# Optimization experiments

Hardware: AMD Instinct MI355X
Metric: run time of the kernel (lower is better)

Reference implementation:

```python
import jax, jax.numpy as jnp
import numpy as np

B, N, IN_DIM, HEADS, OUT_DIM = 8, 2048, 256, 4, 64
NEG_SLOPE = 0.2


def setup_inputs() -> dict:
    key = jax.random.key(0)
    k_h, k_w, k_as, k_ad = jax.random.split(key, 4)
    h = jax.random.normal(k_h, (B, N, IN_DIM), dtype=jnp.float32)
    # xavier-uniform-like scales
    w_lim = float(np.sqrt(6.0 / (IN_DIM + HEADS * OUT_DIM)))
    a_lim = float(np.sqrt(6.0 / (HEADS + OUT_DIM)))
    W = jax.random.uniform(k_w, (IN_DIM, HEADS * OUT_DIM), jnp.float32, -w_lim, w_lim)
    a_src = jax.random.uniform(k_as, (HEADS, OUT_DIM), jnp.float32, -a_lim, a_lim)
    a_dst = jax.random.uniform(k_ad, (HEADS, OUT_DIM), jnp.float32, -a_lim, a_lim)
    bias = jnp.zeros((HEADS * OUT_DIM,), jnp.float32)
    mask = jnp.ones((B, N), dtype=bool)
    return {"h": h, "W": W, "a_src": a_src, "a_dst": a_dst, "bias": bias, "mask": mask}


def reference(h, W, a_src, a_dst, bias, mask):
    Bn, Nn, _ = h.shape
    Hh, Dd = a_src.shape
    # Wh: [B, H, N, D]
    Wh = (h @ W).reshape(Bn, Nn, Hh, Dd).transpose(0, 2, 1, 3)
    el = jnp.einsum("bhnd,hd->bhn", Wh, a_src)  # [B,H,N]
    er = jnp.einsum("bhnd,hd->bhn", Wh, a_dst)  # [B,H,N]
    # e[b,h,i,j] = leaky_relu(el[b,h,i] + er[b,h,j])
    e = jax.nn.leaky_relu(el[..., :, None] + er[..., None, :], NEG_SLOPE)
    e = jnp.where(mask[:, None, None, :], e, jnp.float32(-1e9))
    alpha = jax.nn.softmax(e, axis=-1)  # over source nodes j (dropout=0/eval)
    h_prime = jnp.einsum("bhij,bhjd->bhid", alpha, Wh)  # [B,H,N,D]
    h_prime = h_prime.transpose(0, 2, 1, 3).reshape(Bn, Nn, Hh * Dd)  # concat heads
    return h_prime + bias
```

## Files before the change

kernel.cpp:

```cpp
#include <hip/hip_runtime.h>
#include <math.h>

#define B_   8
#define N_   2048
#define IN_  256
#define H_   4
#define D_   64
#define C_   256
#define M_   (B_*N_)
#define NEG  0.2f
#define LOG2E 1.4426950408889634f

typedef short bf16x8 __attribute__((ext_vector_type(8)));
typedef float f32x4  __attribute__((ext_vector_type(4)));

__device__ inline ushort f32_to_bf16_rne(float x) {
    union { float f; unsigned u; } c; c.f = x;
    unsigned u = c.u + 0x7FFFu + ((c.u >> 16) & 1u);
    return (ushort)(u >> 16);
}
__device__ inline float bf16_hi_to_f32(ushort u) {
    union { unsigned u; float f; } c; c.u = ((unsigned)u) << 16;
    return c.f;
}
__device__ inline void split8(const float v[8], bf16x8* hi, bf16x8* lo) {
    union { bf16x8 v; ushort u[8]; } H, L;
    #pragma unroll
    for (int j = 0; j < 8; j++) {
        ushort hb = f32_to_bf16_rne(v[j]);
        H.u[j] = hb;
        L.u[j] = f32_to_bf16_rne(v[j] - bf16_hi_to_f32(hb));
    }
    *hi = H.v; *lo = L.v;
}

__global__ __launch_bounds__(256) void wprep_kernel(const float* __restrict__ W,
                                                    ushort* __restrict__ Wt_hi,
                                                    ushort* __restrict__ Wt_lo) {
    const int t = threadIdx.x, blk = blockIdx.x;
    ushort his[4], los[4];
    #pragma unroll
    for (int kk = 0; kk < 4; kk++) {
        float v = W[(blk * 4 + kk) * 256 + t];
        ushort hi = f32_to_bf16_rne(v);
        his[kk] = hi;
        los[kk] = f32_to_bf16_rne(v - bf16_hi_to_f32(hi));
    }
    *(uint2*)&Wt_hi[(size_t)t * 256 + blk * 4] =
        make_uint2(((uint)his[0]) | (((uint)his[1]) << 16), ((uint)his[2]) | (((uint)his[3]) << 16));
    *(uint2*)&Wt_lo[(size_t)t * 256 + blk * 4] =
        make_uint2(((uint)los[0]) | (((uint)los[1]) << 16), ((uint)los[2]) | (((uint)los[3]) << 16));
}

#define BP 264
#define EP 136

__global__ __launch_bounds__(256, 2) void gemm_fused(const float* __restrict__ h,
                                                     const ushort* __restrict__ Wt_hi,
                                                     const ushort* __restrict__ Wt_lo,
                                                     const float* __restrict__ a_src,
                                                     const float* __restrict__ a_dst,
                                                     ushort* __restrict__ Wht,
                                                     float* __restrict__ Ee,
                                                     float* __restrict__ Ff,
                                                     float* __restrict__ Gg) {
    __shared__ ushort Bs_h[64 * BP], Bs_l[64 * BP];

    const int t = threadIdx.x;
    const int m0 = blockIdx.x * 128;
    const int nb = blockIdx.y;
    const int b  = m0 >> 11;
    const int wid = t >> 6, lane = t & 63;
    const int c16 = lane & 15, quad = lane >> 4;

    {
        const int c = t >> 2, kq = t & 3;
        const ushort* sh = Wt_hi + (size_t)(nb * 64 + c) * 256 + kq * 64;
        const ushort* sl = Wt_lo + (size_t)(nb * 64 + c) * 256 + kq * 64;
        ushort* dh = &Bs_h[c * BP + kq * 64];
        ushort* dl = &Bs_l[c * BP + kq * 64];
        #pragma unroll
        for (int q = 0; q < 8; q++) {
            *(uint4*)(dh + q * 8) = *(const uint4*)(sh + q * 8);
            *(uint4*)(dl + q * 8) = *(const uint4*)(sl + q * 8);
        }
    }

    const int row0 = m0 + wid * 32 + c16;
    const float* hp0 = h + (size_t)row0 * 256 + quad * 8;
    const float* hp1 = hp0 + 16 * 256;

    float4 p0a = *(const float4*)hp0, p0b = *(const float4*)(hp0 + 4);
    float4 p1a = *(const float4*)hp1, p1b = *(const float4*)(hp1 + 4);

    __syncthreads();

    f32x4 acc[2][4] = {};
    for (int k0 = 0; k0 < 256; k0 += 32) {
        float v0[8] = {p0a.x, p0a.y, p0a.z, p0a.w, p0b.x, p0b.y, p0b.z, p0b.w};
        float v1[8] = {p1a.x, p1a.y, p1a.z, p1a.w, p1b.x, p1b.y, p1b.z, p1b.w};
        if (k0 < 224) {
            p0a = *(const float4*)(hp0 + k0 + 32); p0b = *(const float4*)(hp0 + k0 + 36);
            p1a = *(const float4*)(hp1 + k0 + 32); p1b = *(const float4*)(hp1 + k0 + 36);
        }
        bf16x8 ah0, al0, ah1, al1;
        split8(v0, &ah0, &al0);
        split8(v1, &ah1, &al1);
        #pragma unroll
        for (int fc = 0; fc < 4; fc++) {
            bf16x8 bhf = *(const bf16x8*)&Bs_h[(fc * 16 + c16) * BP + k0 + quad * 8];
            bf16x8 blf = *(const bf16x8*)&Bs_l[(fc * 16 + c16) * BP + k0 + quad * 8];
            acc[0][fc] = __builtin_amdgcn_mfma_f32_16x16x32_bf16(ah0, bhf, acc[0][fc], 0, 0, 0);
            acc[0][fc] = __builtin_amdgcn_mfma_f32_16x16x32_bf16(al0, bhf, acc[0][fc], 0, 0, 0);
            acc[0][fc] = __builtin_amdgcn_mfma_f32_16x16x32_bf16(ah0, blf, acc[0][fc], 0, 0, 0);
            acc[1][fc] = __builtin_amdgcn_mfma_f32_16x16x32_bf16(ah1, bhf, acc[1][fc], 0, 0, 0);
            acc[1][fc] = __builtin_amdgcn_mfma_f32_16x16x32_bf16(al1, bhf, acc[1][fc], 0, 0, 0);
            acc[1][fc] = __builtin_amdgcn_mfma_f32_16x16x32_bf16(ah1, blf, acc[1][fc], 0, 0, 0);
        }
    }

    {
        float avs[4], avd[4];
        #pragma unroll
        for (int fc = 0; fc < 4; fc++) {
            avs[fc] = a_src[nb * 64 + fc * 16 + c16];
            avd[fc] = a_dst[nb * 64 + fc * 16 + c16];
        }
        float ds[2][4] = {}, dd[2][4] = {};
        #pragma unroll
        for (int rw = 0; rw < 2; rw++)
            #pragma unroll
            for (int r = 0; r < 4; r++)
                #pragma unroll
                for (int fc = 0; fc < 4; fc++) {
                    ds[rw][r] += acc[rw][fc][r] * avs[fc];
                    dd[rw][r] += acc[rw][fc][r] * avd[fc];
                }
        #pragma unroll
        for (int off = 1; off < 16; off <<= 1)
            #pragma unroll
            for (int rw = 0; rw < 2; rw++)
                #pragma unroll
                for (int r = 0; r < 4; r++) {
                    ds[rw][r] += __shfl_xor(ds[rw][r], off);
                    dd[rw][r] += __shfl_xor(dd[rw][r], off);
                }
        if (c16 == 0) {
            #pragma unroll
            for (int rw = 0; rw < 2; rw++)
                #pragma unroll
                for (int r = 0; r < 4; r++) {
                    int m = m0 + wid * 32 + rw * 16 + quad * 4 + r;
                    int idx = (b * 4 + nb) * N_ + (m & 2047);
                    float ee = ds[rw][r] * LOG2E;
                    float rr = dd[rw][r] * LOG2E;
                    Ee[idx] = __builtin_amdgcn_exp2f(rr);
                    Ff[idx] = __builtin_amdgcn_exp2f(NEG * rr);
                    Gg[idx] = __builtin_amdgcn_exp2f(-0.8f * ee);
                }
        }
    }

    __syncthreads();
    ushort* Es = Bs_h;
    #pragma unroll
    for (int rw = 0; rw < 2; rw++) {
        const int nloc = wid * 32 + rw * 16 + quad * 4;
        #pragma unroll
        for (int fc = 0; fc < 4; fc++) {
            const int d = fc * 16 + c16;
            uint2 pk = make_uint2(
                ((uint)f32_to_bf16_rne(acc[rw][fc][0])) | (((uint)f32_to_bf16_rne(acc[rw][fc][1])) << 16),
                ((uint)f32_to_bf16_rne(acc[rw][fc][2])) | (((uint)f32_to_bf16_rne(acc[rw][fc][3])) << 16));
            *(uint2*)&Es[d * EP + nloc] = pk;
        }
    }
    __syncthreads();
    {
        const int d = t >> 2, ch = t & 3;
        ushort* dst = Wht + ((size_t)(b * 4 + nb) * 64 + d) * N_ + (m0 & 2047) + ch * 32;
        const ushort* srcl = &Es[d * EP + ch * 32];
        #pragma unroll
        for (int q = 0; q < 4; q++)
            *(uint4*)(dst + q * 8) = *(const uint4*)(srcl + q * 8);
    }
}

#define TPA 80

__global__ __launch_bounds__(256, 2) void attn_kernel(const ushort* __restrict__ Wht,
                                                      const float* __restrict__ Ee,
                                                      const float* __restrict__ Ff,
                                                      const float* __restrict__ Gg,
                                                      const float* __restrict__ bias,
                                                      float* __restrict__ out) {
    __shared__ ushort Whs[2][64 * TPA];
    __shared__ float E_s[2][64], F_s[2][64];
    const int t = threadIdx.x;
    const int bh = blockIdx.x, b = bh >> 2, hh = bh & 3;
    const int wid = t >> 6, lane = t & 63;
    const int c16 = lane & 15, quad = lane >> 4;
    const int ibase = blockIdx.y * 128 + wid * 32;
    const int sd = t >> 3, sch = t & 7;

    float Gi[2];
    #pragma unroll
    for (int g = 0; g < 2; g++) Gi[g] = Gg[bh * N_ + ibase + g * 16 + c16];

    f32x4 acc[2][4] = {};
    f32x4 den[2] = {};
    const bf16x8 ones = {0x3F80, 0x3F80, 0x3F80, 0x3F80,
                         0x3F80, 0x3F80, 0x3F80, 0x3F80};
    const ushort* WhtB = Wht + (size_t)bh * 64 * N_;
    const float* Eb = Ee + (size_t)bh * N_;
    const float* Fb = Ff + (size_t)bh * N_;

    uint4 w0 = *(const uint4*)(WhtB + (size_t)sd * N_ + sch * 8);
    uint4 w1 = *(const uint4*)(WhtB + (size_t)(sd + 32) * N_ + sch * 8);
    float ev_e = 0.f, ev_f = 0.f;
    if (t < 64) { ev_e = Eb[t]; ev_f = Fb[t]; }

    for (int jt = 0; jt < 32; jt++) {
        const int buf = jt & 1;
        *(uint4*)&Whs[buf][sd * TPA + sch * 8]        = w0;
        *(uint4*)&Whs[buf][(sd + 32) * TPA + sch * 8] = w1;
        if (t < 64) { E_s[buf][t] = ev_e; F_s[buf][t] = ev_f; }
        if (jt < 31) {
            const int j1 = (jt + 1) * 64;
            w0 = *(const uint4*)(WhtB + (size_t)sd * N_ + j1 + sch * 8);
            w1 = *(const uint4*)(WhtB + (size_t)(sd + 32) * N_ + j1 + sch * 8);
            if (t < 64) { ev_e = Eb[j1 + t]; ev_f = Fb[j1 + t]; }
        }
        __syncthreads();
        #pragma unroll
        for (int ks = 0; ks < 2; ks++) {
            const int jb = ks * 32 + quad * 8;
            float4 e0 = *(const float4*)&E_s[buf][jb];
            float4 e1 = *(const float4*)&E_s[buf][jb + 4];
            float4 f0 = *(const float4*)&F_s[buf][jb];
            float4 f1 = *(const float4*)&F_s[buf][jb + 4];
            float E8[8] = {e0.x, e0.y, e0.z, e0.w, e1.x, e1.y, e1.z, e1.w};
            float F8[8] = {f0.x, f0.y, f0.z, f0.w, f1.x, f1.y, f1.z, f1.w};
            bf16x8 bfr[4];
            #pragma unroll
            for (int fd = 0; fd < 4; fd++)
                bfr[fd] = *(const bf16x8*)&Whs[buf][(fd * 16 + c16) * TPA + jb];
            #pragma unroll
            for (int g = 0; g < 2; g++) {
                const float gi = Gi[g];
                uint uu[8];
                #pragma unroll
                for (int j = 0; j < 8; j++) {
                    float q = fmaxf(E8[j], gi * F8[j]);
                    uu[j] = __float_as_uint(q) + 0x8000u;
                }
                union { bf16x8 v; uint u[4]; } af;
                #pragma unroll
                for (int j = 0; j < 4; j++)
                    af.u[j] = __builtin_amdgcn_perm(uu[2 * j + 1], uu[2 * j], 0x07060302u);
                #pragma unroll
                for (int fd = 0; fd < 4; fd++)
                    acc[g][fd] = __builtin_amdgcn_mfma_f32_16x16x32_bf16(af.v, bfr[fd], acc[g][fd], 0, 0, 0);
                den[g] = __builtin_amdgcn_mfma_f32_16x16x32_bf16(af.v, ones, den[g], 0, 0, 0);
            }
        }
    }

    float bl[4];
    #pragma unroll
    for (int fd = 0; fd < 4; fd++) bl[fd] = bias[hh * 64 + fd * 16 + c16];
    #pragma unroll
    for (int g = 0; g < 2; g++)
        #pragma unroll
        for (int r = 0; r < 4; r++) {
            int i = ibase + g * 16 + quad * 4 + r;
            float inv = 1.0f / den[g][r];
            float* dst = out + (size_t)(b * N_ + i) * C_ + hh * 64;
            #pragma unroll
            for (int fd = 0; fd < 4; fd++)
                dst[fd * 16 + c16] = acc[g][fd][r] * inv + bl[fd];
        }
}

extern "C" void kernel_launch(void* const* d_in, const int* in_sizes, int n_in,
                              void* d_out, int out_size, void* d_ws, size_t ws_size,
                              hipStream_t stream) {
    const float* h     = (const float*)d_in[0];
    const float* W     = (const float*)d_in[1];
    const float* a_src = (const float*)d_in[2];
    const float* a_dst = (const float*)d_in[3];
    const float* bias  = (const float*)d_in[4];
    float* out = (float*)d_out;

    ushort* Wt_hi = (ushort*)d_ws;
    ushort* Wt_lo = Wt_hi + 256 * 256;
    ushort* Wht   = Wt_lo + 256 * 256;
    float*  Ee    = (float*)(Wht + (size_t)M_ * C_);
    float*  Ff    = Ee + 32 * N_;
    float*  Gg    = Ff + 32 * N_;

    wprep_kernel<<<64, 256, 0, stream>>>(W, Wt_hi, Wt_lo);
    gemm_fused<<<dim3(M_ / 128, 4), 256, 0, stream>>>(h, Wt_hi, Wt_lo, a_src, a_dst,
                                                      Wht, Ee, Ff, Gg);
    attn_kernel<<<dim3(32, 16), 256, 0, stream>>>(Wht, Ee, Ff, Gg, bias, out);
}
```

Before: 122.8 us.

## Replace dense attention with sort-and-prefix-sum evaluation of separable leaky-relu softmax

```diff
diff --git a/kernel.cpp b/kernel.cpp
--- a/kernel.cpp
+++ b/kernel.cpp
@@ -53,17 +53,15 @@
 }
 
 #define BP 264
-#define EP 136
 
 __global__ __launch_bounds__(256, 2) void gemm_fused(const float* __restrict__ h,
                                                      const ushort* __restrict__ Wt_hi,
                                                      const ushort* __restrict__ Wt_lo,
                                                      const float* __restrict__ a_src,
                                                      const float* __restrict__ a_dst,
-                                                     ushort* __restrict__ Wht,
-                                                     float* __restrict__ Ee,
-                                                     float* __restrict__ Ff,
-                                                     float* __restrict__ Gg) {
+                                                     float* __restrict__ Wh,
+                                                     float* __restrict__ eL,
+                                                     float* __restrict__ rL) {
     __shared__ ushort Bs_h[64 * BP], Bs_l[64 * BP];
 
     const int t = threadIdx.x;
@@ -152,134 +150,233 @@
                 for (int r = 0; r < 4; r++) {
                     int m = m0 + wid * 32 + rw * 16 + quad * 4 + r;
                     int idx = (b * 4 + nb) * N_ + (m & 2047);
-                    float ee = ds[rw][r] * LOG2E;
-                    float rr = dd[rw][r] * LOG2E;
-                    Ee[idx] = __builtin_amdgcn_exp2f(rr);
-                    Ff[idx] = __builtin_amdgcn_exp2f(NEG * rr);
-                    Gg[idx] = __builtin_amdgcn_exp2f(-0.8f * ee);
+                    eL[idx] = ds[rw][r] * LOG2E;
+                    rL[idx] = dd[rw][r] * LOG2E;
                 }
         }
     }
 
+    #pragma unroll
+    for (int rw = 0; rw < 2; rw++)
+        #pragma unroll
+        for (int r = 0; r < 4; r++) {
+            int n = m0 + wid * 32 + rw * 16 + quad * 4 + r;
+            float* dst = Wh + (size_t)n * 256 + nb * 64;
+            #pragma unroll
+            for (int fc = 0; fc < 4; fc++)
+                dst[fc * 16 + c16] = acc[rw][fc][r];
+        }
+}
+
+__global__ __launch_bounds__(256) void sort_kernel(const float* __restrict__ rL,
+                                                   float* __restrict__ r_srt,
+                                                   int* __restrict__ perm,
+                                                   float* __restrict__ E_srt,
+                                                   float* __restrict__ F_srt) {
+    __shared__ float key[2048];
+    __shared__ int   idx[2048];
+    const int bh = blockIdx.x, t = threadIdx.x;
+    for (int s = t; s < 2048; s += 256) { key[s] = rL[bh * 2048 + s]; idx[s] = s; }
     __syncthreads();
-    ushort* Es = Bs_h;
-    #pragma unroll
-    for (int rw = 0; rw < 2; rw++) {
-        const int nloc = wid * 32 + rw * 16 + quad * 4;
-        #pragma unroll
-        for (int fc = 0; fc < 4; fc++) {
-            const int d = fc * 16 + c16;
-            uint2 pk = make_uint2(
-                ((uint)f32_to_bf16_rne(acc[rw][fc][0])) | (((uint)f32_to_bf16_rne(acc[rw][fc][1])) << 16),
-                ((uint)f32_to_bf16_rne(acc[rw][fc][2])) | (((uint)f32_to_bf16_rne(acc[rw][fc][3])) << 16));
-            *(uint2*)&Es[d * EP + nloc] = pk;
-        }
-    }
+    for (int k = 2; k <= 2048; k <<= 1) {
+        for (int j = k >> 1; j > 0; j >>= 1) {
+            for (int s = t; s < 2048; s += 256) {
+                int p = s ^ j;
+                if (p > s) {
+                    bool up = ((s & k) == 0);
+                    float a = key[s], bq = key[p];
+                    bool sw = up ? (a > bq) : (a < bq);
+                    if (sw) {
+                        key[s] = bq; key[p] = a;
+                        int ia = idx[s]; idx[s] = idx[p]; idx[p] = ia;
+                    }
+                }
+            }
+            __syncthreads();
+        }
+    }
+    for (int s = t; s < 2048; s += 256) {
+        float rv = key[s];
+        r_srt[bh * 2048 + s] = rv;
+        perm[bh * 2048 + s]  = idx[s];
+        E_srt[bh * 2048 + s] = __builtin_amdgcn_exp2f(rv);
+        F_srt[bh * 2048 + s] = __builtin_amdgcn_exp2f(NEG * rv);
+    }
+}
+
+__global__ __launch_bounds__(256) void chunksum_kernel(const float* __restrict__ Wh,
+                                                       const int* __restrict__ perm,
+                                                       const float* __restrict__ E_srt,
+                                                       const float* __restrict__ F_srt,
+                                                       float* __restrict__ chunkF,
+                                                       float* __restrict__ chunkE,
+                                                       float* __restrict__ chunk_sf,
+                                                       float* __restrict__ chunk_se) {
+    const int bh = blockIdx.x;
+    const int b = bh >> 2, hh = bh & 3;
+    const int w = threadIdx.x >> 6, lane = threadIdx.x & 63;
+    const int ch = blockIdx.y * 4 + w;
+    const int j0 = ch * 32;
+
+    float fv = 0.f, ev = 0.f; int pv = 0;
+    if (lane < 32) {
+        fv = F_srt[bh * 2048 + j0 + lane];
+        ev = E_srt[bh * 2048 + j0 + lane];
+        pv = perm[bh * 2048 + j0 + lane];
+    }
+    float v[32];
+    #pragma unroll
+    for (int jj = 0; jj < 32; jj++) {
+        int pj = __shfl(pv, jj);
+        v[jj] = Wh[((size_t)(b * 2048 + pj)) * 256 + hh * 64 + lane];
+    }
+    float aF = 0.f, aE = 0.f, sf = 0.f, se = 0.f;
+    #pragma unroll
+    for (int jj = 0; jj < 32; jj++) {
+        float fj = __shfl(fv, jj), ej = __shfl(ev, jj);
+        aF += fj * v[jj]; aE += ej * v[jj];
+        sf += fj; se += ej;
+    }
+    size_t o = ((size_t)bh * 64 + ch) * 64 + lane;
+    chunkF[o] = aF; chunkE[o] = aE;
+    if (lane == 0) { chunk_sf[bh * 64 + ch] = sf; chunk_se[bh * 64 + ch] = se; }
+}
+
+__global__ __launch_bounds__(64) void scan_kernel(const float* __restrict__ chunkF,
+                                                  const float* __restrict__ chunkE,
+                                                  const float* __restrict__ chunk_sf,
+                                                  const float* __restrict__ chunk_se,
+                                                  float* __restrict__ offF,
+                                                  float* __restrict__ offE,
+                                                  float* __restrict__ offF_s,
+                                                  float* __restrict__ offE_s,
+                                                  float* __restrict__ PF,
+                                                  float* __restrict__ SES,
+                                                  float* __restrict__ pf_s,
+                                                  float* __restrict__ ses_s) {
+    const int bh = blockIdx.x, d = threadIdx.x;
+    float accF = 0.f, sF = 0.f;
+    for (int c = 0; c < 64; c++) {
+        size_t o = ((size_t)bh * 64 + c) * 64 + d;
+        offF[o] = accF;
+        if (d == 0) offF_s[bh * 64 + c] = sF;
+        accF += chunkF[o];
+        sF += chunk_sf[bh * 64 + c];
+    }
+    float accE = 0.f, sE = 0.f;
+    for (int c = 63; c >= 0; c--) {
+        size_t o = ((size_t)bh * 64 + c) * 64 + d;
+        offE[o] = accE;
+        if (d == 0) offE_s[bh * 64 + c] = sE;
+        accE += chunkE[o];
+        sE += chunk_se[bh * 64 + c];
+    }
+    PF[((size_t)bh * 2049 + 2048) * 64 + d]  = accF;
+    SES[((size_t)bh * 2049 + 2048) * 64 + d] = 0.0f;
+    if (d == 0) { pf_s[bh * 2049 + 2048] = sF; ses_s[bh * 2049 + 2048] = 0.0f; }
+}
+
+__global__ __launch_bounds__(64) void emit_kernel(const float* __restrict__ Wh,
+                                                  const int* __restrict__ perm,
+                                                  const float* __restrict__ E_srt,
+                                                  const float* __restrict__ F_srt,
+                                                  const float* __restrict__ offF,
+                                                  const float* __restrict__ offE,
+                                                  const float* __restrict__ offF_s,
+                                                  const float* __restrict__ offE_s,
+                                                  float* __restrict__ PF,
+                                                  float* __restrict__ SES,
+                                                  float* __restrict__ pf_s,
+                                                  float* __restrict__ ses_s) {
+    const int bh = blockIdx.x, ch = blockIdx.y;
+    const int b = bh >> 2, hh = bh & 3;
+    const int d = threadIdx.x;
+    const int j0 = ch * 32;
+
+    float fv = 0.f, ev = 0.f; int pv = 0;
+    if (d < 32) {
+        fv = F_srt[bh * 2048 + j0 + d];
+        ev = E_srt[bh * 2048 + j0 + d];
+        pv = perm[bh * 2048 + j0 + d];
+    }
+    float v[32];
+    #pragma unroll
+    for (int jj = 0; jj < 32; jj++) {
+        int pj = __shfl(pv, jj);
+        v[jj] = Wh[((size_t)(b * 2048 + pj)) * 256 + hh * 64 + d];
+    }
+    float accF = offF[((size_t)bh * 64 + ch) * 64 + d];
+    float sF   = offF_s[bh * 64 + ch];
+    #pragma unroll
+    for (int jj = 0; jj < 32; jj++) {
+        float fj = __shfl(fv, jj);
+        size_t ro = ((size_t)bh * 2049 + j0 + jj) * 64 + d;
+        PF[ro] = accF;
+        if (d == 0) pf_s[bh * 2049 + j0 + jj] = sF;
+        accF += fj * v[jj];
+        sF += fj;
+    }
+    float accE = offE[((size_t)bh * 64 + ch) * 64 + d];
+    float sE   = offE_s[bh * 64 + ch];
+    #pragma unroll
+    for (int jj = 31; jj >= 0; jj--) {
+        float ej = __shfl(ev, jj);
+        accE += ej * v[jj];
+        sE += ej;
+        size_t ro = ((size_t)bh * 2049 + j0 + jj) * 64 + d;
+        SES[ro] = accE;
+        if (d == 0) ses_s[bh * 2049 + j0 + jj] = sE;
+    }
+}
+
+__global__ __launch_bounds__(256) void final_kernel(const float* __restrict__ eL,
+                                                    const float* __restrict__ r_srt,
+                                                    const float* __restrict__ PF,
+                                                    const float* __restrict__ SES,
+                                                    const float* __restrict__ pf_s,
+                                                    const float* __restrict__ ses_s,
+                                                    const float* __restrict__ bias,
+                                                    float* __restrict__ out) {
+    __shared__ float r_sh[2048];
+    __shared__ int   t_sh[64];
+    __shared__ float g_sh[64];
+    const int bh = blockIdx.x, ig = blockIdx.y;
+    const int b = bh >> 2, hh = bh & 3;
+    const int t = threadIdx.x;
+
+    for (int s = t; s < 2048; s += 256) r_sh[s] = r_srt[bh * 2048 + s];
     __syncthreads();
-    {
-        const int d = t >> 2, ch = t & 3;
-        ushort* dst = Wht + ((size_t)(b * 4 + nb) * 64 + d) * N_ + (m0 & 2047) + ch * 32;
-        const ushort* srcl = &Es[d * EP + ch * 32];
-        #pragma unroll
-        for (int q = 0; q < 4; q++)
-            *(uint4*)(dst + q * 8) = *(const uint4*)(srcl + q * 8);
-    }
-}
-
-#define TPA 80
-
-__global__ __launch_bounds__(256, 2) void attn_kernel(const ushort* __restrict__ Wht,
-                                                      const float* __restrict__ Ee,
-                                                      const float* __restrict__ Ff,
-                                                      const float* __restrict__ Gg,
-                                                      const float* __restrict__ bias,
-                                                      float* __restrict__ out) {
-    __shared__ ushort Whs[2][64 * TPA];
-    __shared__ float E_s[2][64], F_s[2][64];
-    const int t = threadIdx.x;
-    const int bh = blockIdx.x, b = bh >> 2, hh = bh & 3;
-    const int wid = t >> 6, lane = t & 63;
-    const int c16 = lane & 15, quad = lane >> 4;
-    const int ibase = blockIdx.y * 128 + wid * 32;
-    const int sd = t >> 3, sch = t & 7;
-
-    float Gi[2];
-    #pragma unroll
-    for (int g = 0; g < 2; g++) Gi[g] = Gg[bh * N_ + ibase + g * 16 + c16];
-
-    f32x4 acc[2][4] = {};
-    f32x4 den[2] = {};
-    const bf16x8 ones = {0x3F80, 0x3F80, 0x3F80, 0x3F80,
-                         0x3F80, 0x3F80, 0x3F80, 0x3F80};
-    const ushort* WhtB = Wht + (size_t)bh * 64 * N_;
-    const float* Eb = Ee + (size_t)bh * N_;
-    const float* Fb = Ff + (size_t)bh * N_;
-
-    uint4 w0 = *(const uint4*)(WhtB + (size_t)sd * N_ + sch * 8);
-    uint4 w1 = *(const uint4*)(WhtB + (size_t)(sd + 32) * N_ + sch * 8);
-    float ev_e = 0.f, ev_f = 0.f;
-    if (t < 64) { ev_e = Eb[t]; ev_f = Fb[t]; }
-
-    for (int jt = 0; jt < 32; jt++) {
-        const int buf = jt & 1;
-        *(uint4*)&Whs[buf][sd * TPA + sch * 8]        = w0;
-        *(uint4*)&Whs[buf][(sd + 32) * TPA + sch * 8] = w1;
-        if (t < 64) { E_s[buf][t] = ev_e; F_s[buf][t] = ev_f; }
-        if (jt < 31) {
-            const int j1 = (jt + 1) * 64;
-            w0 = *(const uint4*)(WhtB + (size_t)sd * N_ + j1 + sch * 8);
-            w1 = *(const uint4*)(WhtB + (size_t)(sd + 32) * N_ + j1 + sch * 8);
-            if (t < 64) { ev_e = Eb[j1 + t]; ev_f = Fb[j1 + t]; }
-        }
-        __syncthreads();
-        #pragma unroll
-        for (int ks = 0; ks < 2; ks++) {
-            const int jb = ks * 32 + quad * 8;
-            float4 e0 = *(const float4*)&E_s[buf][jb];
-            float4 e1 = *(const float4*)&E_s[buf][jb + 4];
-            float4 f0 = *(const float4*)&F_s[buf][jb];
-            float4 f1 = *(const float4*)&F_s[buf][jb + 4];
-            float E8[8] = {e0.x, e0.y, e0.z, e0.w, e1.x, e1.y, e1.z, e1.w};
-            float F8[8] = {f0.x, f0.y, f0.z, f0.w, f1.x, f1.y, f1.z, f1.w};
-            bf16x8 bfr[4];
-            #pragma unroll
-            for (int fd = 0; fd < 4; fd++)
-                bfr[fd] = *(const bf16x8*)&Whs[buf][(fd * 16 + c16) * TPA + jb];
-            #pragma unroll
-            for (int g = 0; g < 2; g++) {
-                const float gi = Gi[g];
-                uint uu[8];
-                #pragma unroll
-                for (int j = 0; j < 8; j++) {
-                    float q = fmaxf(E8[j], gi * F8[j]);
-                    uu[j] = __float_as_uint(q) + 0x8000u;
-                }
-                union { bf16x8 v; uint u[4]; } af;
-                #pragma unroll
-                for (int j = 0; j < 4; j++)
-                    af.u[j] = __builtin_amdgcn_perm(uu[2 * j + 1], uu[2 * j], 0x07060302u);
-                #pragma unroll
-                for (int fd = 0; fd < 4; fd++)
-                    acc[g][fd] = __builtin_amdgcn_mfma_f32_16x16x32_bf16(af.v, bfr[fd], acc[g][fd], 0, 0, 0);
-                den[g] = __builtin_amdgcn_mfma_f32_16x16x32_bf16(af.v, ones, den[g], 0, 0, 0);
-            }
-        }
-    }
-
-    float bl[4];
-    #pragma unroll
-    for (int fd = 0; fd < 4; fd++) bl[fd] = bias[hh * 64 + fd * 16 + c16];
-    #pragma unroll
-    for (int g = 0; g < 2; g++)
-        #pragma unroll
-        for (int r = 0; r < 4; r++) {
-            int i = ibase + g * 16 + quad * 4 + r;
-            float inv = 1.0f / den[g][r];
-            float* dst = out + (size_t)(b * N_ + i) * C_ + hh * 64;
-            #pragma unroll
-            for (int fd = 0; fd < 4; fd++)
-                dst[fd * 16 + c16] = acc[g][fd][r] * inv + bl[fd];
-        }
+    if (t < 64) {
+        int i = ig * 64 + t;
+        float e = eL[bh * 2048 + i];
+        float target = -e;
+        int lo = 0, hi = 2048;
+        while (lo < hi) {
+            int mid = (lo + hi) >> 1;
+            if (r_sh[mid] < target) lo = mid + 1; else hi = mid;
+        }
+        t_sh[t] = lo;
+        g_sh[t] = __builtin_amdgcn_exp2f(-0.8f * e);
+    }
+    __syncthreads();
+
+    const int w = t >> 6, lane = t & 63;
+    const float bl = bias[hh * 64 + lane];
+    #pragma unroll 4
+    for (int q = 0; q < 16; q++) {
+        int il = w * 16 + q;
+        int ti = t_sh[il];
+        float G = g_sh[il];
+        size_t base = ((size_t)bh * 2049 + ti) * 64 + lane;
+        float pf  = PF[base];
+        float ses = SES[base];
+        float dpf  = pf_s[bh * 2049 + ti];
+        float dses = ses_s[bh * 2049 + ti];
+        float num = G * pf + ses;
+        float den = G * dpf + dses;
+        int i = ig * 64 + il;
+        out[((size_t)(b * 2048 + i)) * 256 + hh * 64 + lane] = num / den + bl;
+    }
 }
 
 extern "C" void kernel_launch(void* const* d_in, const int* in_sizes, int n_in,
@@ -292,15 +389,40 @@
     const float* bias  = (const float*)d_in[4];
     float* out = (float*)d_out;
 
-    ushort* Wt_hi = (ushort*)d_ws;
-    ushort* Wt_lo = Wt_hi + 256 * 256;
-    ushort* Wht   = Wt_lo + 256 * 256;
-    float*  Ee    = (float*)(Wht + (size_t)M_ * C_);
-    float*  Ff    = Ee + 32 * N_;
-    float*  Gg    = Ff + 32 * N_;
+    float* Wh       = (float*)d_ws;
+    float* eL       = Wh + (size_t)M_ * C_;
+    float* rL       = eL + 32 * N_;
+    float* r_srt    = rL + 32 * N_;
+    float* E_srt    = r_srt + 32 * N_;
+    float* F_srt    = E_srt + 32 * N_;
+    float* chunkF   = F_srt + 32 * N_;
+    float* chunkE   = chunkF + 32 * 64 * 64;
+    float* chunk_sf = chunkE + 32 * 64 * 64;
+    float* chunk_se = chunk_sf + 32 * 64;
+    float* offF     = chunk_se + 32 * 64;
+    float* offE     = offF + 32 * 64 * 64;
+    float* offF_s   = offE + 32 * 64 * 64;
+    float* offE_s   = offF_s + 32 * 64;
+    float* PF       = offE_s + 32 * 64;
+    float* SES      = PF + (size_t)32 * 2049 * 64;
+    float* pf_s     = SES + (size_t)32 * 2049 * 64;
+    float* ses_s    = pf_s + 32 * 2049;
+    int*   perm     = (int*)(ses_s + 32 * 2049);
+    ushort* Wt_hi   = (ushort*)(perm + 32 * N_);
+    ushort* Wt_lo   = Wt_hi + 256 * 256;
 
     wprep_kernel<<<64, 256, 0, stream>>>(W, Wt_hi, Wt_lo);
     gemm_fused<<<dim3(M_ / 128, 4), 256, 0, stream>>>(h, Wt_hi, Wt_lo, a_src, a_dst,
-                                                      Wht, Ee, Ff, Gg);
-    attn_kernel<<<dim3(32, 16), 256, 0, stream>>>(Wht, Ee, Ff, Gg, bias, out);
-}
+                                                      Wh, eL, rL);
+    sort_kernel<<<32, 256, 0, stream>>>(rL, r_srt, perm, E_srt, F_srt);
+    chunksum_kernel<<<dim3(32, 16), 256, 0, stream>>>(Wh, perm, E_srt, F_srt,
+                                                      chunkF, chunkE, chunk_sf, chunk_se);
+    scan_kernel<<<32, 64, 0, stream>>>(chunkF, chunkE, chunk_sf, chunk_se,
+                                       offF, offE, offF_s, offE_s,
+                                       PF, SES, pf_s, ses_s);
+    emit_kernel<<<dim3(32, 64), 64, 0, stream>>>(Wh, perm, E_srt, F_srt,
+                                                 offF, offE, offF_s, offE_s,
+                                                 PF, SES, pf_s, ses_s);
+    final_kernel<<<dim3(32, 32), 256, 0, stream>>>(eL, r_srt, PF, SES, pf_s, ses_s,
+                                                   bias, out);
+}
```

After: 230.3 us. +87.5%, slower.
